# Kernel optimization log

Hardware: AMD Instinct MI355X
Metric: run time of the kernel (lower is better)

## Reference

```python
import jax, jax.numpy as jnp
import numpy as np

MSA_DIM = 256
N_HEADS = 8
HEAD_DIM = MSA_DIM // N_HEADS
PAIR_DIM = 128
SCALE = 1.0 / float(np.sqrt(HEAD_DIM))


def setup_inputs() -> dict:
    key = jax.random.key(0)
    ks = jax.random.split(key, 7)
    B, S, L = 1, 128, 384
    return {
        "msa": jax.random.normal(ks[0], (B, S, L, MSA_DIM), dtype=jnp.float32),
        "pair": jax.random.normal(ks[1], (B, L, L, PAIR_DIM), dtype=jnp.float32),
        "Wq": jax.random.normal(ks[2], (MSA_DIM, MSA_DIM), dtype=jnp.float32) * 0.02,
        "Wk": jax.random.normal(ks[3], (MSA_DIM, MSA_DIM), dtype=jnp.float32) * 0.02,
        "Wv": jax.random.normal(ks[4], (MSA_DIM, MSA_DIM), dtype=jnp.float32) * 0.02,
        "Wo": jax.random.normal(ks[5], (MSA_DIM, MSA_DIM), dtype=jnp.float32) * 0.02,
        "Wpb": jax.random.normal(ks[6], (N_HEADS, PAIR_DIM), dtype=jnp.float32) * 0.02,
    }


def reference(msa, pair, Wq, Wk, Wv, Wo, Wpb):
    B, S, L, D = msa.shape
    H, hd = N_HEADS, HEAD_DIM
    # projections (nn.Linear: y = x @ W.T), split heads -> (B,S,H,L,hd)
    q = (msa @ Wq.T).reshape(B, S, L, H, hd)
    k = (msa @ Wk.T).reshape(B, S, L, H, hd)
    v = (msa @ Wv.T).reshape(B, S, L, H, hd)
    # NOTE: faithful to the original forward — pair_bias is computed but the
    # Triton kernel performs plain flash attention, so the bias is NOT added.
    _pair_bias = jnp.einsum('bijp,hp->bhij', pair, Wpb)  # dead code, as in source
    # attention logits per MSA row: (B,S,H,L,L)
    scores = jnp.einsum('bslhd,bsmhd->bshlm', q, k) * SCALE
    attn = jax.nn.softmax(scores, axis=-1)
    out = jnp.einsum('bshlm,bsmhd->bslhd', attn, v).reshape(B, S, L, D)
    return out @ Wo.T
```

## Files before the change

### kernel.cpp

```cpp
#include <hip/hip_runtime.h>
#include <stdint.h>

typedef unsigned short u16;
typedef __bf16 bf16x8 __attribute__((ext_vector_type(8)));
typedef short s16x4 __attribute__((ext_vector_type(4)));
typedef float f32x4 __attribute__((ext_vector_type(4)));

#define QKV_STRIDE 12288

__device__ __forceinline__ u16 f2bf(float x) {
    unsigned int u = __float_as_uint(x);
    u += 0x7fffu + ((u >> 16) & 1u);
    return (u16)(u >> 16);
}
__device__ __forceinline__ float bf2f(u16 h) {
    return __uint_as_float(((unsigned int)h) << 16);
}

__device__ __forceinline__ void async_copy16(const u16* g, u16* l) {
    __builtin_amdgcn_global_load_lds(
        (const __attribute__((address_space(1))) unsigned int*)g,
        (__attribute__((address_space(3))) unsigned int*)l, 16, 0, 0);
}

__global__ void prep(const float* __restrict__ msa,
                     const float* __restrict__ Wq, const float* __restrict__ Wk,
                     const float* __restrict__ Wv, const float* __restrict__ Wo,
                     u16* __restrict__ msa_bf, u16* __restrict__ Wqkv,
                     u16* __restrict__ Woh, u16* __restrict__ Wol) {
    int b = blockIdx.x;
    if (b < 12288) {
        int i = b * 256 + threadIdx.x;
        float4 v = ((const float4*)msa)[i];
        ushort4 o;
        o.x = f2bf(v.x); o.y = f2bf(v.y); o.z = f2bf(v.z); o.w = f2bf(v.w);
        ((ushort4*)msa_bf)[i] = o;
    } else {
        int i = (b - 12288) * 256 + threadIdx.x;
        Wqkv[i]          = f2bf(Wq[i]);
        Wqkv[65536 + i]  = f2bf(Wk[i]);
        Wqkv[131072 + i] = f2bf(Wv[i]);
        float w = Wo[i];
        u16 hi = f2bf(w);
        Woh[i] = hi;
        Wol[i] = f2bf(w - bf2f(hi));
    }
}

__launch_bounds__(256, 4)
__global__ void qkv_gemm(const u16* __restrict__ A, const u16* __restrict__ W,
                         u16* __restrict__ Qb, u16* __restrict__ Kb, u16* __restrict__ VTb) {
    __shared__ __align__(16) u16 As[2 * 128 * 32];
    __shared__ __align__(16) u16 Bs[2 * 128 * 32];
    const int tid = threadIdx.x;
    const int tm = blockIdx.x % 384, tn = blockIdx.x / 384;
    const bool trans = (tn < 4);
    const int lane = tid & 63, wave = tid >> 6;
    const int lm = lane & 15, lq = lane >> 4;
    const int wm = (wave >> 1) * 64, wn = (wave & 1) * 64;
    const float CEXPF = 0.17677669529663687f * 1.4426950408889634f;
    f32x4 acc[4][4] = {};

    const int srow = wave * 16 + (lane >> 2);
    const int scol = (lane & 3) * 8;
    const int ldso = wave * 512 + lane * 8;
    const u16* gA0 = &A[(tm * 128 + srow) * 256 + scol];
    const u16* gA1 = &A[(tm * 128 + 64 + srow) * 256 + scol];
    const u16* gB0 = &W[(tn * 128 + srow) * 256 + scol];
    const u16* gB1 = &W[(tn * 128 + 64 + srow) * 256 + scol];

    async_copy16(gA0, &As[ldso]);
    async_copy16(gA1, &As[2048 + ldso]);
    async_copy16(gB0, &Bs[ldso]);
    async_copy16(gB1, &Bs[2048 + ldso]);
    __syncthreads();

    #pragma unroll
    for (int t = 0; t < 8; ++t) {
        const int p = (t & 1) * 4096;
        if (t < 7) {
            const int pn = ((t + 1) & 1) * 4096;
            const int k1 = (t + 1) * 32;
            async_copy16(gA0 + k1, &As[pn + ldso]);
            async_copy16(gA1 + k1, &As[pn + 2048 + ldso]);
            async_copy16(gB0 + k1, &Bs[pn + ldso]);
            async_copy16(gB1 + k1, &Bs[pn + 2048 + ldso]);
        }
        const u16* Xs = trans ? &Bs[p] : &As[p];
        const u16* Ys = trans ? &As[p] : &Bs[p];
        bf16x8 xf[4], yf[4];
        #pragma unroll
        for (int i = 0; i < 4; ++i)
            xf[i] = *(const bf16x8*)&Xs[(wm + i * 16 + lm) * 32 + lq * 8];
        #pragma unroll
        for (int j = 0; j < 4; ++j)
            yf[j] = *(const bf16x8*)&Ys[(wn + j * 16 + lm) * 32 + lq * 8];
        #pragma unroll
        for (int i = 0; i < 4; ++i)
            #pragma unroll
            for (int j = 0; j < 4; ++j)
                acc[i][j] = __builtin_amdgcn_mfma_f32_16x16x32_bf16(xf[i], yf[j], acc[i][j], 0, 0, 0);
        if (t < 7) __syncthreads();
    }

    if (trans) {
        #pragma unroll
        for (int i = 0; i < 4; ++i) {
            int F0 = tn * 128 + wm + i * 16 + lq * 4;
            int which = F0 >> 8;
            int h = (F0 >> 5) & 7, d0 = F0 & 31;
            u16* dst = which ? Kb : Qb;
            float scale = which ? 1.0f : CEXPF;
            #pragma unroll
            for (int j = 0; j < 4; ++j) {
                int R = tm * 128 + wn + j * 16 + lm;
                int s = R / 384, l = R - s * 384;
                ushort4 o;
                o.x = f2bf(acc[i][j][0] * scale);
                o.y = f2bf(acc[i][j][1] * scale);
                o.z = f2bf(acc[i][j][2] * scale);
                o.w = f2bf(acc[i][j][3] * scale);
                *(ushort4*)&dst[((s * 8 + h) * 384 + l) * 32 + d0] = o;
            }
        }
    } else {
        #pragma unroll
        for (int j = 0; j < 4; ++j) {
            int F = tn * 128 + wn + j * 16 + lm;
            int h = (F >> 5) & 7, d = F & 31;
            #pragma unroll
            for (int i = 0; i < 4; ++i) {
                int R0 = tm * 128 + wm + i * 16 + lq * 4;
                int s = R0 / 384, l0 = R0 - s * 384;
                ushort4 o;
                o.x = f2bf(acc[i][j][0]);
                o.y = f2bf(acc[i][j][1]);
                o.z = f2bf(acc[i][j][2]);
                o.w = f2bf(acc[i][j][3]);
                *(ushort4*)&VTb[((s * 8 + h) * 32 + d) * 384 + l0] = o;
            }
        }
    }
}

__launch_bounds__(256, 6)
__global__ void msa_attention(const u16* __restrict__ Qb, const u16* __restrict__ Kb,
                              const u16* __restrict__ VTb,
                              u16* __restrict__ Ahi, u16* __restrict__ Alo) {
    __shared__ __align__(16) u16 Vt[32 * 392];
    const int tid = threadIdx.x;
    const int bid = blockIdx.x;
    const int xcd = bid & 7, j = bid >> 3;
    const int jd3 = j / 3;
    const int sh = xcd * 128 + jd3, lpart = j - jd3 * 3;
    const int s = sh >> 3, h = sh & 7;
    const u16* Qg = Qb + (size_t)sh * QKV_STRIDE;
    const u16* Kg = Kb + (size_t)sh * QKV_STRIDE;
    const u16* Vg = VTb + (size_t)sh * QKV_STRIDE;

    for (int i = tid; i < 1536; i += 256) {
        int d = i / 48, c = i - d * 48;
        *(uint4*)&Vt[d * 392 + c * 8] = *(const uint4*)&Vg[d * 384 + c * 8];
    }

    const int lane = tid & 63, wave = tid >> 6;
    const int lm = lane & 15, lq = lane >> 4;

    bf16x8 aq[2];
    #pragma unroll
    for (int it = 0; it < 2; ++it) {
        int l = lpart * 128 + (wave * 2 + it) * 16 + lm;
        aq[it] = *(const bf16x8*)&Qg[l * 32 + lq * 8];
    }
    __syncthreads();

    f32x4 o[2][2] = {};
    f32x4 lacc[2] = {};
    union pack8 { s16x4 h[2]; bf16x8 v; };
    pack8 ones8;
    {
        s16x4 one4 = {(short)0x3F80, (short)0x3F80, (short)0x3F80, (short)0x3F80};
        ones8.h[0] = one4; ones8.h[1] = one4;
    }

    for (int n0 = 0; n0 < 384; n0 += 32) {
        bf16x8 kf0 = *(const bf16x8*)&Kg[(n0 + lm) * 32 + lq * 8];
        bf16x8 kf1 = *(const bf16x8*)&Kg[(n0 + 16 + lm) * 32 + lq * 8];
        pack8 va0, va1;
        va0.h[0] = *(const s16x4*)&Vt[lm * 392 + n0 + lq * 4];
        va0.h[1] = *(const s16x4*)&Vt[lm * 392 + n0 + 16 + lq * 4];
        va1.h[0] = *(const s16x4*)&Vt[(16 + lm) * 392 + n0 + lq * 4];
        va1.h[1] = *(const s16x4*)&Vt[(16 + lm) * 392 + n0 + 16 + lq * 4];
        #pragma unroll
        for (int it = 0; it < 2; ++it) {
            f32x4 z = {0.f, 0.f, 0.f, 0.f};
            f32x4 s0 = __builtin_amdgcn_mfma_f32_16x16x32_bf16(kf0, aq[it], z, 0, 0, 0);
            f32x4 s1 = __builtin_amdgcn_mfma_f32_16x16x32_bf16(kf1, aq[it], z, 0, 0, 0);
            float p0[4], p1[4];
            #pragma unroll
            for (int r = 0; r < 4; ++r) {
                p0[r] = __builtin_amdgcn_exp2f(s0[r]);
                p1[r] = __builtin_amdgcn_exp2f(s1[r]);
            }
            pack8 pb;
            union { s16x4 v; uint2 u; } pk0, pk1;
            pk0.u.x = __builtin_amdgcn_perm(__float_as_uint(p0[1]), __float_as_uint(p0[0]), 0x07060302u);
            pk0.u.y = __builtin_amdgcn_perm(__float_as_uint(p0[3]), __float_as_uint(p0[2]), 0x07060302u);
            pk1.u.x = __builtin_amdgcn_perm(__float_as_uint(p1[1]), __float_as_uint(p1[0]), 0x07060302u);
            pk1.u.y = __builtin_amdgcn_perm(__float_as_uint(p1[3]), __float_as_uint(p1[2]), 0x07060302u);
            pb.h[0] = pk0.v; pb.h[1] = pk1.v;
            o[it][0] = __builtin_amdgcn_mfma_f32_16x16x32_bf16(va0.v, pb.v, o[it][0], 0, 0, 0);
            o[it][1] = __builtin_amdgcn_mfma_f32_16x16x32_bf16(va1.v, pb.v, o[it][1], 0, 0, 0);
            lacc[it] = __builtin_amdgcn_mfma_f32_16x16x32_bf16(ones8.v, pb.v, lacc[it], 0, 0, 0);
        }
    }

    #pragma unroll
    for (int it = 0; it < 2; ++it) {
        float inv = __builtin_amdgcn_rcpf(lacc[it][0]);
        int l = lpart * 128 + (wave * 2 + it) * 16 + lm;
        int base = (s * 384 + l) * 256 + h * 32 + lq * 4;
        #pragma unroll
        for (int dt = 0; dt < 2; ++dt) {
            ushort4 oh, ol;
            float x0 = o[it][dt][0] * inv, x1 = o[it][dt][1] * inv;
            float x2 = o[it][dt][2] * inv, x3 = o[it][dt][3] * inv;
            oh.x = f2bf(x0); ol.x = f2bf(x0 - bf2f(oh.x));
            oh.y = f2bf(x1); ol.y = f2bf(x1 - bf2f(oh.y));
            oh.z = f2bf(x2); ol.z = f2bf(x2 - bf2f(oh.z));
            oh.w = f2bf(x3); ol.w = f2bf(x3 - bf2f(oh.w));
            *(ushort4*)&Ahi[base + dt * 16] = oh;
            *(ushort4*)&Alo[base + dt * 16] = ol;
        }
    }
}

__launch_bounds__(256, 2)
__global__ void out_gemm(const u16* __restrict__ Ahi, const u16* __restrict__ Alo,
                         const u16* __restrict__ Woh, const u16* __restrict__ Wol,
                         float* __restrict__ out) {
    __shared__ __align__(16) u16 Ah[2 * 128 * 32], Al[2 * 128 * 32];
    __shared__ __align__(16) u16 Bh[2 * 128 * 32], Bl[2 * 128 * 32];
    const int tid = threadIdx.x;
    const int tm = blockIdx.x % 384, tn = blockIdx.x / 384;
    const int lane = tid & 63, wave = tid >> 6;
    const int lm = lane & 15, lq = lane >> 4;
    const int wm = (wave >> 1) * 64, wn = (wave & 1) * 64;
    f32x4 acc[4][4] = {};

    const int srow = wave * 16 + (lane >> 2);
    const int scol = (lane & 3) * 8;
    const int lo0 = wave * 512 + lane * 8, lo1 = 2048 + wave * 512 + lane * 8;
    const u16* gAh0 = &Ahi[(tm * 128 + srow) * 256 + scol];
    const u16* gAh1 = &Ahi[(tm * 128 + 64 + srow) * 256 + scol];
    const u16* gAl0 = &Alo[(tm * 128 + srow) * 256 + scol];
    const u16* gAl1 = &Alo[(tm * 128 + 64 + srow) * 256 + scol];
    const u16* gBh0 = &Woh[(tn * 128 + srow) * 256 + scol];
    const u16* gBh1 = &Woh[(tn * 128 + 64 + srow) * 256 + scol];
    const u16* gBl0 = &Wol[(tn * 128 + srow) * 256 + scol];
    const u16* gBl1 = &Wol[(tn * 128 + 64 + srow) * 256 + scol];

    async_copy16(gAh0, &Ah[lo0]);
    async_copy16(gAh1, &Ah[lo1]);
    async_copy16(gAl0, &Al[lo0]);
    async_copy16(gAl1, &Al[lo1]);
    async_copy16(gBh0, &Bh[lo0]);
    async_copy16(gBh1, &Bh[lo1]);
    async_copy16(gBl0, &Bl[lo0]);
    async_copy16(gBl1, &Bl[lo1]);
    __syncthreads();

    #pragma unroll
    for (int t = 0; t < 8; ++t) {
        const int p = (t & 1) * 4096;
        if (t < 7) {
            const int pn = ((t + 1) & 1) * 4096;
            const int k1 = (t + 1) * 32;
            async_copy16(gAh0 + k1, &Ah[pn + lo0]);
            async_copy16(gAh1 + k1, &Ah[pn + lo1]);
            async_copy16(gAl0 + k1, &Al[pn + lo0]);
            async_copy16(gAl1 + k1, &Al[pn + lo1]);
            async_copy16(gBh0 + k1, &Bh[pn + lo0]);
            async_copy16(gBh1 + k1, &Bh[pn + lo1]);
            async_copy16(gBl0 + k1, &Bl[pn + lo0]);
            async_copy16(gBl1 + k1, &Bl[pn + lo1]);
        }
        bf16x8 whf[4], wlf[4], ahf[4], alf[4];
        #pragma unroll
        for (int i = 0; i < 4; ++i) {
            whf[i] = *(const bf16x8*)&Bh[p + (wm + i * 16 + lm) * 32 + lq * 8];
            wlf[i] = *(const bf16x8*)&Bl[p + (wm + i * 16 + lm) * 32 + lq * 8];
        }
        #pragma unroll
        for (int j = 0; j < 4; ++j) {
            ahf[j] = *(const bf16x8*)&Ah[p + (wn + j * 16 + lm) * 32 + lq * 8];
            alf[j] = *(const bf16x8*)&Al[p + (wn + j * 16 + lm) * 32 + lq * 8];
        }
        #pragma unroll
        for (int i = 0; i < 4; ++i)
            #pragma unroll
            for (int j = 0; j < 4; ++j) {
                acc[i][j] = __builtin_amdgcn_mfma_f32_16x16x32_bf16(whf[i], alf[j], acc[i][j], 0, 0, 0);
                acc[i][j] = __builtin_amdgcn_mfma_f32_16x16x32_bf16(wlf[i], ahf[j], acc[i][j], 0, 0, 0);
                acc[i][j] = __builtin_amdgcn_mfma_f32_16x16x32_bf16(whf[i], ahf[j], acc[i][j], 0, 0, 0);
            }
        if (t < 7) __syncthreads();
    }
    #pragma unroll
    for (int i = 0; i < 4; ++i) {
        int F0 = tn * 128 + wm + i * 16 + lq * 4;
        #pragma unroll
        for (int j = 0; j < 4; ++j) {
            int R = tm * 128 + wn + j * 16 + lm;
            *(f32x4*)&out[R * 256 + F0] = acc[i][j];
        }
    }
}

extern "C" void kernel_launch(void* const* d_in, const int* in_sizes, int n_in,
                              void* d_out, int out_size, void* d_ws, size_t ws_size,
                              hipStream_t stream) {
    const float* msa = (const float*)d_in[0];
    const float* Wq = (const float*)d_in[2];
    const float* Wk = (const float*)d_in[3];
    const float* Wv = (const float*)d_in[4];
    const float* Wo = (const float*)d_in[5];
    char* ws = (char*)d_ws;
    u16* msa_bf = (u16*)(ws + 0);
    u16* Qb     = (u16*)(ws + 25165824);
    u16* Kb     = (u16*)(ws + 50331648);
    u16* VTb    = (u16*)(ws + 75497472);
    u16* Ahi    = (u16*)(ws + 100663296);
    u16* Alo    = (u16*)(ws + 125829120);
    u16* Wqkv   = (u16*)(ws + 150994944);
    u16* Woh    = (u16*)(ws + 151388160);
    u16* Wol    = (u16*)(ws + 151519232);
    float* out  = (float*)d_out;

    hipLaunchKernelGGL(prep, dim3(12544), dim3(256), 0, stream, msa, Wq, Wk, Wv, Wo,
                       msa_bf, Wqkv, Woh, Wol);
    hipLaunchKernelGGL(qkv_gemm, dim3(2304), dim3(256), 0, stream, msa_bf, Wqkv, Qb, Kb, VTb);
    hipLaunchKernelGGL(msa_attention, dim3(3072), dim3(256), 0, stream, Qb, Kb, VTb, Ahi, Alo);
    hipLaunchKernelGGL(out_gemm, dim3(768), dim3(256), 0, stream, Ahi, Alo, Woh, Wol, out);
}
```

Before: 266.8 us.

## Triple-buffer QKV GEMM LDS loads with partial vmcnt waits

```diff
diff --git a/kernel.cpp b/kernel.cpp
--- a/kernel.cpp
+++ b/kernel.cpp
@@ -47,11 +47,11 @@
     }
 }
 
-__launch_bounds__(256, 4)
+__launch_bounds__(256, 2)
 __global__ void qkv_gemm(const u16* __restrict__ A, const u16* __restrict__ W,
                          u16* __restrict__ Qb, u16* __restrict__ Kb, u16* __restrict__ VTb) {
-    __shared__ __align__(16) u16 As[2 * 128 * 32];
-    __shared__ __align__(16) u16 Bs[2 * 128 * 32];
+    __shared__ __align__(16) u16 As[3 * 128 * 32];
+    __shared__ __align__(16) u16 Bs[3 * 128 * 32];
     const int tid = threadIdx.x;
     const int tm = blockIdx.x % 384, tn = blockIdx.x / 384;
     const bool trans = (tn < 4);
@@ -69,23 +69,25 @@
     const u16* gB0 = &W[(tn * 128 + srow) * 256 + scol];
     const u16* gB1 = &W[(tn * 128 + 64 + srow) * 256 + scol];
 
-    async_copy16(gA0, &As[ldso]);
-    async_copy16(gA1, &As[2048 + ldso]);
-    async_copy16(gB0, &Bs[ldso]);
-    async_copy16(gB1, &Bs[2048 + ldso]);
-    __syncthreads();
+    #define STAGE(t, b) do {                                      \
+        const int _k = (t) * 32, _o = (b) * 4096 + ldso;          \
+        async_copy16(gA0 + _k, &As[_o]);                          \
+        async_copy16(gA1 + _k, &As[_o + 2048]);                   \
+        async_copy16(gB0 + _k, &Bs[_o]);                          \
+        async_copy16(gB1 + _k, &Bs[_o + 2048]);                   \
+    } while (0)
+
+    STAGE(0, 0);
+    STAGE(1, 1);
+    __builtin_amdgcn_sched_barrier(0);
+    asm volatile("s_waitcnt vmcnt(4)" ::: "memory");
+    __builtin_amdgcn_s_barrier();
 
     #pragma unroll
     for (int t = 0; t < 8; ++t) {
-        const int p = (t & 1) * 4096;
-        if (t < 7) {
-            const int pn = ((t + 1) & 1) * 4096;
-            const int k1 = (t + 1) * 32;
-            async_copy16(gA0 + k1, &As[pn + ldso]);
-            async_copy16(gA1 + k1, &As[pn + 2048 + ldso]);
-            async_copy16(gB0 + k1, &Bs[pn + ldso]);
-            async_copy16(gB1 + k1, &Bs[pn + 2048 + ldso]);
-        }
+        if (t < 6) STAGE(t + 2, (t + 2) % 3);
+        __builtin_amdgcn_sched_barrier(0);
+        const int p = (t % 3) * 4096;
         const u16* Xs = trans ? &Bs[p] : &As[p];
         const u16* Ys = trans ? &As[p] : &Bs[p];
         bf16x8 xf[4], yf[4];
@@ -100,8 +102,17 @@
             #pragma unroll
             for (int j = 0; j < 4; ++j)
                 acc[i][j] = __builtin_amdgcn_mfma_f32_16x16x32_bf16(xf[i], yf[j], acc[i][j], 0, 0, 0);
-        if (t < 7) __syncthreads();
-    }
+        if (t < 6) {
+            __builtin_amdgcn_sched_barrier(0);
+            asm volatile("s_waitcnt vmcnt(4)" ::: "memory");
+            __builtin_amdgcn_s_barrier();
+        } else if (t == 6) {
+            __builtin_amdgcn_sched_barrier(0);
+            asm volatile("s_waitcnt vmcnt(0)" ::: "memory");
+            __builtin_amdgcn_s_barrier();
+        }
+    }
+    #undef STAGE
 
     if (trans) {
         #pragma unroll
```

Result: no change. 267.4 us (+0.2%).
